# Performance work log

Measured on AMD Instinct MI355X. Metric: run time of the kernel, lower is better.

Reference implementation:

```python
import jax, jax.numpy as jnp
import numpy as np

N_NODES = 100000
N_EDGES = 640000
N_LABEL = 100000
IN_C, HID_C, OUT_C = 128, 128, 64


def setup_inputs() -> dict:
    key = jax.random.key(0)
    ks = jax.random.split(key, 9)
    x = jax.random.normal(ks[0], (N_NODES, IN_C), dtype=jnp.float32)
    edge_index = jax.random.randint(ks[1], (2, N_EDGES), 0, N_NODES, dtype=jnp.int64)
    edge_label_index = jax.random.randint(ks[2], (2, N_LABEL), 0, N_NODES, dtype=jnp.int64)
    s = 0.05  # small init scale
    # PyG SAGEConv: lin_l applied to mean-aggregated neighbors (with bias), lin_r to root (no bias)
    W1l = jax.random.normal(ks[3], (HID_C, IN_C), dtype=jnp.float32) * s
    b1 = jnp.zeros((HID_C,), dtype=jnp.float32)
    W1r = jax.random.normal(ks[4], (HID_C, IN_C), dtype=jnp.float32) * s
    W2l = jax.random.normal(ks[5], (OUT_C, HID_C), dtype=jnp.float32) * s
    b2 = jnp.zeros((OUT_C,), dtype=jnp.float32)
    W2r = jax.random.normal(ks[6], (OUT_C, HID_C), dtype=jnp.float32) * s
    return {"x": x, "edge_index": edge_index, "edge_label_index": edge_label_index,
            "W1l": W1l, "b1": b1, "W1r": W1r, "W2l": W2l, "b2": b2, "W2r": W2r}


def _sage_conv(x, src, dst, Wl, b, Wr):
    # mean aggregation of source features at destination nodes
    agg = jax.ops.segment_sum(x[src], dst, num_segments=N_NODES)  # [N, d]
    cnt = jax.ops.segment_sum(jnp.ones((src.shape[0],), x.dtype), dst, num_segments=N_NODES)
    mean = agg / jnp.maximum(cnt, 1.0)[:, None]
    return mean @ Wl.T + b + x @ Wr.T


def reference(x, edge_index, edge_label_index, W1l, b1, W1r, W2l, b2, W2r):
    src, dst = edge_index[0], edge_index[1]
    h = jax.nn.relu(_sage_conv(x, src, dst, W1l, b1, W1r))
    z = _sage_conv(h, src, dst, W2l, b2, W2r)
    # edge-wise dot-product decode
    scores = jnp.sum(z[edge_label_index[0]] * z[edge_label_index[1]], axis=-1)  # [E_label]
    return scores
```

## Files before the change

### kernel.cpp

```cpp
#include <hip/hip_runtime.h>

#define N_NODES 100000
#define N_EDGES 640000
#define N_LABEL 100000
#define CAP 32

typedef __bf16 bf16x8 __attribute__((ext_vector_type(8)));
typedef float f32x4 __attribute__((ext_vector_type(4)));

#define CW1L 0
#define CB1  16384
#define CW1R 16512
#define CW2L 32896
#define CB2  41088
#define CW2R 41152
#define NWTS 49344

#define NB_W 193
#define NB_X 12500

__device__ __forceinline__ float bf2f(unsigned short u) {
    union { unsigned int i; float f; } c; c.i = ((unsigned int)u) << 16; return c.f;
}
__device__ __forceinline__ unsigned short f2bf(float f) {
    union { float f; unsigned int i; } c; c.f = f;
    unsigned int lsb = (c.i >> 16) & 1u;
    c.i += 0x7fffu + lsb;
    return (unsigned short)(c.i >> 16);
}

__global__ void k_detect(const unsigned int* __restrict__ xw,
                         const unsigned int* __restrict__ eiw,
                         int* __restrict__ flags) {
    int l = threadIdx.x;
    unsigned int w = xw[l];
    unsigned short lo = (unsigned short)(w & 0xffffu);
    int e = (lo >> 7) & 0xff;
    bool bf_like = (lo == 0) || (e >= 98 && e <= 138);
    unsigned long long m = __ballot(bf_like);
    unsigned int ew = eiw[2 * l + 1];
    unsigned long long mz = __ballot(ew == 0u);
    if (l == 0) {
        flags[0] = (__popcll(m) < 48) ? 1 : 0;
        flags[1] = (__popcll(mz) == 64) ? 1 : 0;
    }
}

__global__ void k_convwx(const void* W1l, const void* b1, const void* W1r,
                         const void* W2l, const void* b2, const void* W2r,
                         unsigned short* __restrict__ wts,
                         const void* __restrict__ x, unsigned short* __restrict__ xb,
                         const int* __restrict__ flags) {
    int b = blockIdx.x;
    int f32m = flags[0];
    if (b < NB_W) {
        int i = b * 256 + threadIdx.x;
        if (i >= NWTS) return;
        const void* src; int local;
        if      (i < CB1)  { src = W1l; local = i; }
        else if (i < CW1R) { src = b1;  local = i - CB1; }
        else if (i < CW2L) { src = W1r; local = i - CW1R; }
        else if (i < CB2)  { src = W2l; local = i - CW2L; }
        else if (i < CW2R) { src = b2;  local = i - CB2; }
        else               { src = W2r; local = i - CW2R; }
        wts[i] = f32m ? f2bf(((const float*)src)[local]) : ((const unsigned short*)src)[local];
    } else {
        int i = (b - NB_W) * 256 + threadIdx.x;
        if (i >= N_NODES * 32) return;
        if (f32m) {
            float4 p = ((const float4*)x)[i];
            ushort4 o;
            o.x = f2bf(p.x); o.y = f2bf(p.y); o.z = f2bf(p.z); o.w = f2bf(p.w);
            ((ushort4*)xb)[i] = o;
        } else {
            ((ushort4*)xb)[i] = ((const ushort4*)x)[i];
        }
    }
}

__global__ void k_fill(const int* __restrict__ ei, int* __restrict__ cnt,
                       int* __restrict__ csr, const int* __restrict__ flags) {
    int e = blockIdx.x * blockDim.x + threadIdx.x;
    if (e >= N_EDGES) return;
    int i64 = flags[1];
    int src = ei[e << i64], dst = ei[(N_EDGES + e) << i64];
    int pos = atomicAdd(&cnt[dst], 1);
    if (pos < CAP) csr[dst * CAP + pos] = src;
}

__global__ __launch_bounds__(256) void k_gemm1f(
    const int* __restrict__ cnt, const int* __restrict__ csr,
    const unsigned short* __restrict__ xb, const unsigned short* __restrict__ wts,
    unsigned short* __restrict__ h)
{
    __shared__ unsigned short smean[32][136];
    int wave = threadIdx.x >> 6, lane = threadIdx.x & 63;
    int nb0 = blockIdx.x * 32;

    int nA = nb0 + wave * 8;
    int half = lane >> 5, sl = lane & 31;
    int rows[4];
#pragma unroll
    for (int p = 0; p < 4; ++p)
        rows[p] = csr[(size_t)(nA + p * 2 + half) * CAP + sl];
    int dpre = (lane < 8) ? cnt[nA + lane] : 0;
    int c2 = lane << 1;

#pragma unroll
    for (int j = 0; j < 8; ++j) {
        int deg = __shfl(dpre, j);
        int m = deg < CAP ? deg : CAP;
        float s0 = 0.f, s1 = 0.f;
        for (int e0 = 0; e0 < m; e0 += 8) {
            unsigned int v[8];
#pragma unroll
            for (int u = 0; u < 8; ++u) {
                int e = e0 + u;
                int sidx = __shfl(rows[j >> 1], (j & 1) * 32 + e);
                sidx = (e < m) ? sidx : 0;
                v[u] = *(const unsigned int*)(xb + (size_t)sidx * 128 + c2);
            }
#pragma unroll
            for (int u = 0; u < 8; ++u) {
                bool ok = (e0 + u) < m;
                s0 += ok ? bf2f((unsigned short)(v[u] & 0xffffu)) : 0.f;
                s1 += ok ? bf2f((unsigned short)(v[u] >> 16)) : 0.f;
            }
        }
        float inv = 1.0f / (deg > 1 ? (float)deg : 1.0f);
        unsigned int o = (unsigned int)f2bf(s0 * inv) | ((unsigned int)f2bf(s1 * inv) << 16);
        *(unsigned int*)&smean[wave * 8 + j][c2] = o;
    }
    __syncthreads();

    int qq = wave;
    int row = lane & 15, kq = lane >> 4;
    bf16x8 Wf[16];
#pragma unroll
    for (int t = 0; t < 2; ++t)
#pragma unroll
        for (int ks = 0; ks < 8; ++ks) {
            const int k0 = ks * 32;
            const unsigned short* base = wts + (k0 < 128 ? CW1L : CW1R)
                + (size_t)(qq * 32 + t * 16 + row) * 128 + (k0 & 127) + kq * 8;
            Wf[t * 8 + ks] = *reinterpret_cast<const bf16x8*>(base);
        }
    int col = lane & 15, rq = lane >> 4;
    float bias0 = bf2f(wts[CB1 + qq * 32 + col]);
    float bias1 = bf2f(wts[CB1 + qq * 32 + 16 + col]);

#pragma unroll
    for (int i = 0; i < 2; ++i) {
        int n0 = nb0 + i * 16;
        bf16x8 Af[8];
#pragma unroll
        for (int ks = 0; ks < 4; ++ks)
            Af[ks] = *reinterpret_cast<const bf16x8*>(&smean[i * 16 + row][ks * 32 + kq * 8]);
        const unsigned short* rx = xb + (size_t)(n0 + row) * 128 + kq * 8;
#pragma unroll
        for (int ks = 0; ks < 4; ++ks)
            Af[4 + ks] = *reinterpret_cast<const bf16x8*>(rx + ks * 32);
        f32x4 acc0 = (f32x4){0.f, 0.f, 0.f, 0.f};
        f32x4 acc1 = (f32x4){0.f, 0.f, 0.f, 0.f};
#pragma unroll
        for (int ks = 0; ks < 8; ++ks) {
            acc0 = __builtin_amdgcn_mfma_f32_16x16x32_bf16(Af[ks], Wf[ks],     acc0, 0, 0, 0);
            acc1 = __builtin_amdgcn_mfma_f32_16x16x32_bf16(Af[ks], Wf[8 + ks], acc1, 0, 0, 0);
        }
#pragma unroll
        for (int r = 0; r < 4; ++r) {
            int n = n0 + rq * 4 + r;
            float v0 = acc0[r] + bias0; v0 = v0 > 0.f ? v0 : 0.f;
            float v1 = acc1[r] + bias1; v1 = v1 > 0.f ? v1 : 0.f;
            h[(size_t)n * 128 + qq * 32 + col]      = f2bf(v0);
            h[(size_t)n * 128 + qq * 32 + 16 + col] = f2bf(v1);
        }
    }
}

__global__ __launch_bounds__(256) void k_gemm2(
    const unsigned short* __restrict__ h, const unsigned short* __restrict__ wts,
    unsigned short* __restrict__ tb)
{
    int w = (int)((blockIdx.x * blockDim.x + threadIdx.x) >> 6);
    int lane = threadIdx.x & 63;
    int q = w & 3;
    int tg = w >> 2;
    int row = lane & 15, kq = lane >> 4;

    const size_t wbase = (q < 2) ? (CW2L + (size_t)(q * 32) * 128)
                                 : (CW2R + (size_t)((q - 2) * 32) * 128);
    bf16x8 Wf[8];
#pragma unroll
    for (int t = 0; t < 2; ++t)
#pragma unroll
        for (int ks = 0; ks < 4; ++ks)
            Wf[t * 4 + ks] = *reinterpret_cast<const bf16x8*>(
                wts + wbase + (size_t)(t * 16 + row) * 128 + ks * 32 + kq * 8);

    int col = lane & 15, rq = lane >> 4;
    int nt0 = tg * 2;
    bf16x8 Af[2][4];

#define LOAD_A2(tile, buf)                                                            \
    {                                                                                 \
        int n0_ = (tile) * 16;                                                        \
        if (n0_ < N_NODES) {                                                          \
            const unsigned short* rh = h + (size_t)(n0_ + row) * 128 + kq * 8;        \
            _Pragma("unroll")                                                         \
            for (int ks = 0; ks < 4; ++ks)                                            \
                Af[buf][ks] = *reinterpret_cast<const bf16x8*>(rh + ks * 32);         \
        }                                                                             \
    }

    LOAD_A2(nt0, 0);
#pragma unroll
    for (int i = 0; i < 2; ++i) {
        int n0 = (nt0 + i) * 16;
        if (n0 >= N_NODES) continue;
        if (i < 1) LOAD_A2(nt0 + i + 1, (i + 1) & 1);
        f32x4 acc0 = (f32x4){0.f, 0.f, 0.f, 0.f};
        f32x4 acc1 = (f32x4){0.f, 0.f, 0.f, 0.f};
#pragma unroll
        for (int ks = 0; ks < 4; ++ks) {
            acc0 = __builtin_amdgcn_mfma_f32_16x16x32_bf16(Af[i & 1][ks], Wf[ks],     acc0, 0, 0, 0);
            acc1 = __builtin_amdgcn_mfma_f32_16x16x32_bf16(Af[i & 1][ks], Wf[4 + ks], acc1, 0, 0, 0);
        }
#pragma unroll
        for (int r = 0; r < 4; ++r) {
            int n = n0 + rq * 4 + r;
            tb[(size_t)n * 128 + q * 32 + col]      = f2bf(acc0[r]);
            tb[(size_t)n * 128 + q * 32 + 16 + col] = f2bf(acc1[r]);
        }
    }
#undef LOAD_A2
}

__global__ __launch_bounds__(256) void k_agg2c(
    const int* __restrict__ cnt, const int* __restrict__ csr,
    const unsigned short* __restrict__ tb, const unsigned short* __restrict__ wts,
    float* __restrict__ z) {
    int wv = (int)((blockIdx.x * blockDim.x + threadIdx.x) >> 6);
    int n2 = wv * 2;
    if (n2 >= N_NODES) return;
    int lane = threadIdx.x & 63;
    int half = lane >> 5, sl = lane & 31;
    int n = n2 + half;
    int dpre = (lane < 2) ? cnt[n2 + lane] : 0;
    int deg = __shfl(dpre, half);
    int m = deg < CAP ? deg : CAP;
    int mo = __shfl(m, lane ^ 32);
    int mmax = m > mo ? m : mo;
    int srcrow = csr[(size_t)n * CAP + sl];
    int c2 = sl << 1;
    float s0 = 0.f, s1 = 0.f;
    for (int e0 = 0; e0 < mmax; e0 += 8) {
        unsigned int v[8];
#pragma unroll
        for (int u = 0; u < 8; ++u) {
            int e = e0 + u;
            int sidx = __shfl(srcrow, half * 32 + e);
            sidx = (e < m) ? sidx : 0;
            v[u] = *(const unsigned int*)(tb + (size_t)sidx * 128 + c2);
        }
#pragma unroll
        for (int u = 0; u < 8; ++u) {
            bool ok = (e0 + u) < m;
            s0 += ok ? bf2f((unsigned short)(v[u] & 0xffffu)) : 0.f;
            s1 += ok ? bf2f((unsigned short)(v[u] >> 16)) : 0.f;
        }
    }
    float inv = 1.0f / (deg > 1 ? (float)deg : 1.0f);
    unsigned int tr = *(const unsigned int*)(tb + (size_t)n * 128 + 64 + c2);
    unsigned int bb = *(const unsigned int*)(wts + CB2 + c2);
    float2 o;
    o.x = s0 * inv + bf2f((unsigned short)(bb & 0xffffu)) + bf2f((unsigned short)(tr & 0xffffu));
    o.y = s1 * inv + bf2f((unsigned short)(bb >> 16))     + bf2f((unsigned short)(tr >> 16));
    *(float2*)(z + (size_t)n * 64 + c2) = o;
}

__global__ void k_decode(const int* __restrict__ eli, const float* __restrict__ z,
                         void* __restrict__ out, const int* __restrict__ flags) {
    long long t = (long long)blockIdx.x * blockDim.x + threadIdx.x;
    int e = (int)(t >> 4);
    if (e >= N_LABEL) return;
    int f32m = flags[0], i64 = flags[1];
    int q = threadIdx.x & 15;
    int a = eli[e << i64], b = eli[(N_LABEL + e) << i64];
    float4 pa = *(const float4*)(z + (size_t)a * 64 + q * 4);
    float4 pb = *(const float4*)(z + (size_t)b * 64 + q * 4);
    float s = pa.x * pb.x + pa.y * pb.y + pa.z * pb.z + pa.w * pb.w;
#pragma unroll
    for (int off = 1; off < 16; off <<= 1) s += __shfl_xor(s, off);
    if (q == 0) {
        if (f32m) ((float*)out)[e] = s;
        else      ((unsigned short*)out)[e] = f2bf(s);
    }
}

extern "C" void kernel_launch(void* const* d_in, const int* in_sizes, int n_in,
                              void* d_out, int out_size, void* d_ws, size_t ws_size,
                              hipStream_t stream) {
    const void* x   = d_in[0];
    const int*  ei  = (const int*)d_in[1];
    const int*  eli = (const int*)d_in[2];
    const void* W1l = d_in[3];
    const void* b1  = d_in[4];
    const void* W1r = d_in[5];
    const void* W2l = d_in[6];
    const void* b2  = d_in[7];
    const void* W2r = d_in[8];

    char* ws = (char*)d_ws;
    const size_t offFlag = 0;
    const size_t offCnt  = 1024;
    const size_t offWts  = 801024;
    const size_t offCsr  = 1u << 20;
    const size_t offXb   = offCsr + (size_t)N_NODES * CAP * 4;
    const size_t offTb   = offXb  + (size_t)N_NODES * 128 * 2;
    const size_t offHz   = offTb  + (size_t)N_NODES * 128 * 2;

    int*            flags = (int*)(ws + offFlag);
    int*            cnt   = (int*)(ws + offCnt);
    unsigned short* wts   = (unsigned short*)(ws + offWts);
    int*            csr   = (int*)(ws + offCsr);
    unsigned short* xb    = (unsigned short*)(ws + offXb);
    unsigned short* tb    = (unsigned short*)(ws + offTb);
    unsigned short* h     = (unsigned short*)(ws + offHz);

    hipMemsetAsync(ws, 0, 1u << 20, stream);

    k_detect<<<1, 64, 0, stream>>>((const unsigned int*)x, (const unsigned int*)ei, flags);

    k_convwx<<<NB_W + NB_X, 256, 0, stream>>>(W1l, b1, W1r, W2l, b2, W2r, wts, x, xb, flags);

    k_fill<<<(N_EDGES + 255) / 256, 256, 0, stream>>>(ei, cnt, csr, flags);

    k_gemm1f<<<N_NODES / 32, 256, 0, stream>>>(cnt, csr, xb, wts, h);

    k_gemm2<<<3125, 256, 0, stream>>>(h, wts, tb);

    float* z = (float*)(ws + offHz);
    k_agg2c<<<12500, 256, 0, stream>>>(cnt, csr, tb, wts, z);

    {
        long long thr = (long long)N_LABEL * 16;
        k_decode<<<(unsigned)((thr + 255) / 256), 256, 0, stream>>>(eli, z, d_out, flags);
    }
}
```

Before: 259.3 us.

## Fuse layer-1 and layer-2 GEMMs via shared memory; store z as bf16

The layer-1 aggregate+GEMM kernel now also runs the layer-2 projection. The ReLU output h stays in shared memory instead of making a global round trip through a separate GEMM kernel, which removes one launch and a 25 MB write/read. z is now stored in bf16 instead of fp32, halving the gather traffic in the decode kernel, which now uses 8 lanes per label edge. The bf16 unpacking is also simplified with mask and shift casts. The cost is lower precision for z and more registers held across the extra syncs in the fused kernel.

```diff
diff --git a/kernel.cpp b/kernel.cpp
--- a/kernel.cpp
+++ b/kernel.cpp
@@ -21,6 +21,9 @@
 
 __device__ __forceinline__ float bf2f(unsigned short u) {
     union { unsigned int i; float f; } c; c.i = ((unsigned int)u) << 16; return c.f;
+}
+__device__ __forceinline__ float asf(unsigned int u) {
+    union { unsigned int i; float f; } c; c.i = u; return c.f;
 }
 __device__ __forceinline__ unsigned short f2bf(float f) {
     union { float f; unsigned int i; } c; c.f = f;
@@ -88,158 +91,141 @@
     if (pos < CAP) csr[dst * CAP + pos] = src;
 }
 
-__global__ __launch_bounds__(256) void k_gemm1f(
+__global__ __launch_bounds__(256) void k_fused1(
     const int* __restrict__ cnt, const int* __restrict__ csr,
     const unsigned short* __restrict__ xb, const unsigned short* __restrict__ wts,
-    unsigned short* __restrict__ h)
+    unsigned short* __restrict__ tb)
 {
-    __shared__ unsigned short smean[32][136];
+    __shared__ unsigned short sm[32][136];
     int wave = threadIdx.x >> 6, lane = threadIdx.x & 63;
     int nb0 = blockIdx.x * 32;
 
-    int nA = nb0 + wave * 8;
-    int half = lane >> 5, sl = lane & 31;
-    int rows[4];
-#pragma unroll
-    for (int p = 0; p < 4; ++p)
-        rows[p] = csr[(size_t)(nA + p * 2 + half) * CAP + sl];
-    int dpre = (lane < 8) ? cnt[nA + lane] : 0;
-    int c2 = lane << 1;
-
-#pragma unroll
-    for (int j = 0; j < 8; ++j) {
-        int deg = __shfl(dpre, j);
-        int m = deg < CAP ? deg : CAP;
-        float s0 = 0.f, s1 = 0.f;
-        for (int e0 = 0; e0 < m; e0 += 8) {
-            unsigned int v[8];
-#pragma unroll
-            for (int u = 0; u < 8; ++u) {
-                int e = e0 + u;
-                int sidx = __shfl(rows[j >> 1], (j & 1) * 32 + e);
-                sidx = (e < m) ? sidx : 0;
-                v[u] = *(const unsigned int*)(xb + (size_t)sidx * 128 + c2);
-            }
-#pragma unroll
-            for (int u = 0; u < 8; ++u) {
-                bool ok = (e0 + u) < m;
-                s0 += ok ? bf2f((unsigned short)(v[u] & 0xffffu)) : 0.f;
-                s1 += ok ? bf2f((unsigned short)(v[u] >> 16)) : 0.f;
-            }
-        }
-        float inv = 1.0f / (deg > 1 ? (float)deg : 1.0f);
-        unsigned int o = (unsigned int)f2bf(s0 * inv) | ((unsigned int)f2bf(s1 * inv) << 16);
-        *(unsigned int*)&smean[wave * 8 + j][c2] = o;
+    {
+        int nA = nb0 + wave * 8;
+        int half = lane >> 5, sl = lane & 31;
+        int rows[4];
+#pragma unroll
+        for (int p = 0; p < 4; ++p)
+            rows[p] = csr[(size_t)(nA + p * 2 + half) * CAP + sl];
+        int dpre = (lane < 8) ? cnt[nA + lane] : 0;
+        int c2 = lane << 1;
+
+#pragma unroll
+        for (int j = 0; j < 8; ++j) {
+            int deg = __shfl(dpre, j);
+            int m = deg < CAP ? deg : CAP;
+            float s0 = 0.f, s1 = 0.f;
+            for (int e0 = 0; e0 < m; e0 += 8) {
+                unsigned int v[8];
+#pragma unroll
+                for (int u = 0; u < 8; ++u) {
+                    int e = e0 + u;
+                    int sidx = __shfl(rows[j >> 1], (j & 1) * 32 + e);
+                    sidx = (e < m) ? sidx : 0;
+                    v[u] = *(const unsigned int*)(xb + (size_t)sidx * 128 + c2);
+                }
+#pragma unroll
+                for (int u = 0; u < 8; ++u) {
+                    unsigned int w = ((e0 + u) < m) ? v[u] : 0u;
+                    s0 += asf(w << 16);
+                    s1 += asf(w & 0xffff0000u);
+                }
+            }
+            float inv = 1.0f / (deg > 1 ? (float)deg : 1.0f);
+            unsigned int o = (unsigned int)f2bf(s0 * inv) | ((unsigned int)f2bf(s1 * inv) << 16);
+            *(unsigned int*)&sm[wave * 8 + j][c2] = o;
+        }
     }
     __syncthreads();
 
     int qq = wave;
     int row = lane & 15, kq = lane >> 4;
-    bf16x8 Wf[16];
-#pragma unroll
-    for (int t = 0; t < 2; ++t)
-#pragma unroll
-        for (int ks = 0; ks < 8; ++ks) {
-            const int k0 = ks * 32;
-            const unsigned short* base = wts + (k0 < 128 ? CW1L : CW1R)
-                + (size_t)(qq * 32 + t * 16 + row) * 128 + (k0 & 127) + kq * 8;
-            Wf[t * 8 + ks] = *reinterpret_cast<const bf16x8*>(base);
-        }
     int col = lane & 15, rq = lane >> 4;
-    float bias0 = bf2f(wts[CB1 + qq * 32 + col]);
-    float bias1 = bf2f(wts[CB1 + qq * 32 + 16 + col]);
-
-#pragma unroll
-    for (int i = 0; i < 2; ++i) {
-        int n0 = nb0 + i * 16;
-        bf16x8 Af[8];
-#pragma unroll
-        for (int ks = 0; ks < 4; ++ks)
-            Af[ks] = *reinterpret_cast<const bf16x8*>(&smean[i * 16 + row][ks * 32 + kq * 8]);
-        const unsigned short* rx = xb + (size_t)(n0 + row) * 128 + kq * 8;
-#pragma unroll
-        for (int ks = 0; ks < 4; ++ks)
-            Af[4 + ks] = *reinterpret_cast<const bf16x8*>(rx + ks * 32);
-        f32x4 acc0 = (f32x4){0.f, 0.f, 0.f, 0.f};
-        f32x4 acc1 = (f32x4){0.f, 0.f, 0.f, 0.f};
-#pragma unroll
-        for (int ks = 0; ks < 8; ++ks) {
-            acc0 = __builtin_amdgcn_mfma_f32_16x16x32_bf16(Af[ks], Wf[ks],     acc0, 0, 0, 0);
-            acc1 = __builtin_amdgcn_mfma_f32_16x16x32_bf16(Af[ks], Wf[8 + ks], acc1, 0, 0, 0);
-        }
-#pragma unroll
-        for (int r = 0; r < 4; ++r) {
-            int n = n0 + rq * 4 + r;
-            float v0 = acc0[r] + bias0; v0 = v0 > 0.f ? v0 : 0.f;
-            float v1 = acc1[r] + bias1; v1 = v1 > 0.f ? v1 : 0.f;
-            h[(size_t)n * 128 + qq * 32 + col]      = f2bf(v0);
-            h[(size_t)n * 128 + qq * 32 + 16 + col] = f2bf(v1);
-        }
-    }
-}
-
-__global__ __launch_bounds__(256) void k_gemm2(
-    const unsigned short* __restrict__ h, const unsigned short* __restrict__ wts,
-    unsigned short* __restrict__ tb)
-{
-    int w = (int)((blockIdx.x * blockDim.x + threadIdx.x) >> 6);
-    int lane = threadIdx.x & 63;
-    int q = w & 3;
-    int tg = w >> 2;
-    int row = lane & 15, kq = lane >> 4;
-
-    const size_t wbase = (q < 2) ? (CW2L + (size_t)(q * 32) * 128)
-                                 : (CW2R + (size_t)((q - 2) * 32) * 128);
-    bf16x8 Wf[8];
-#pragma unroll
-    for (int t = 0; t < 2; ++t)
-#pragma unroll
-        for (int ks = 0; ks < 4; ++ks)
-            Wf[t * 4 + ks] = *reinterpret_cast<const bf16x8*>(
-                wts + wbase + (size_t)(t * 16 + row) * 128 + ks * 32 + kq * 8);
-
-    int col = lane & 15, rq = lane >> 4;
-    int nt0 = tg * 2;
-    bf16x8 Af[2][4];
-
-#define LOAD_A2(tile, buf)                                                            \
-    {                                                                                 \
-        int n0_ = (tile) * 16;                                                        \
-        if (n0_ < N_NODES) {                                                          \
-            const unsigned short* rh = h + (size_t)(n0_ + row) * 128 + kq * 8;        \
-            _Pragma("unroll")                                                         \
-            for (int ks = 0; ks < 4; ++ks)                                            \
-                Af[buf][ks] = *reinterpret_cast<const bf16x8*>(rh + ks * 32);         \
-        }                                                                             \
-    }
-
-    LOAD_A2(nt0, 0);
-#pragma unroll
-    for (int i = 0; i < 2; ++i) {
-        int n0 = (nt0 + i) * 16;
-        if (n0 >= N_NODES) continue;
-        if (i < 1) LOAD_A2(nt0 + i + 1, (i + 1) & 1);
-        f32x4 acc0 = (f32x4){0.f, 0.f, 0.f, 0.f};
-        f32x4 acc1 = (f32x4){0.f, 0.f, 0.f, 0.f};
-#pragma unroll
-        for (int ks = 0; ks < 4; ++ks) {
-            acc0 = __builtin_amdgcn_mfma_f32_16x16x32_bf16(Af[i & 1][ks], Wf[ks],     acc0, 0, 0, 0);
-            acc1 = __builtin_amdgcn_mfma_f32_16x16x32_bf16(Af[i & 1][ks], Wf[4 + ks], acc1, 0, 0, 0);
-        }
-#pragma unroll
-        for (int r = 0; r < 4; ++r) {
-            int n = n0 + rq * 4 + r;
-            tb[(size_t)n * 128 + q * 32 + col]      = f2bf(acc0[r]);
-            tb[(size_t)n * 128 + q * 32 + 16 + col] = f2bf(acc1[r]);
-        }
-    }
-#undef LOAD_A2
+    f32x4 acc[2][2];
+    {
+        bf16x8 Wf[16];
+#pragma unroll
+        for (int t = 0; t < 2; ++t)
+#pragma unroll
+            for (int ks = 0; ks < 8; ++ks) {
+                const int k0 = ks * 32;
+                const unsigned short* base = wts + (k0 < 128 ? CW1L : CW1R)
+                    + (size_t)(qq * 32 + t * 16 + row) * 128 + (k0 & 127) + kq * 8;
+                Wf[t * 8 + ks] = *reinterpret_cast<const bf16x8*>(base);
+            }
+#pragma unroll
+        for (int i = 0; i < 2; ++i) {
+            bf16x8 Af[8];
+#pragma unroll
+            for (int ks = 0; ks < 4; ++ks)
+                Af[ks] = *reinterpret_cast<const bf16x8*>(&sm[i * 16 + row][ks * 32 + kq * 8]);
+            const unsigned short* rx = xb + (size_t)(nb0 + i * 16 + row) * 128 + kq * 8;
+#pragma unroll
+            for (int ks = 0; ks < 4; ++ks)
+                Af[4 + ks] = *reinterpret_cast<const bf16x8*>(rx + ks * 32);
+            acc[i][0] = (f32x4){0.f, 0.f, 0.f, 0.f};
+            acc[i][1] = (f32x4){0.f, 0.f, 0.f, 0.f};
+#pragma unroll
+            for (int ks = 0; ks < 8; ++ks) {
+                acc[i][0] = __builtin_amdgcn_mfma_f32_16x16x32_bf16(Af[ks], Wf[ks],     acc[i][0], 0, 0, 0);
+                acc[i][1] = __builtin_amdgcn_mfma_f32_16x16x32_bf16(Af[ks], Wf[8 + ks], acc[i][1], 0, 0, 0);
+            }
+        }
+    }
+    __syncthreads();
+    {
+        float bias0 = bf2f(wts[CB1 + qq * 32 + col]);
+        float bias1 = bf2f(wts[CB1 + qq * 32 + 16 + col]);
+#pragma unroll
+        for (int i = 0; i < 2; ++i)
+#pragma unroll
+            for (int r = 0; r < 4; ++r) {
+                int nl = i * 16 + rq * 4 + r;
+                float v0 = acc[i][0][r] + bias0; v0 = v0 > 0.f ? v0 : 0.f;
+                float v1 = acc[i][1][r] + bias1; v1 = v1 > 0.f ? v1 : 0.f;
+                sm[nl][qq * 32 + col]      = f2bf(v0);
+                sm[nl][qq * 32 + 16 + col] = f2bf(v1);
+            }
+    }
+    __syncthreads();
+
+    {
+        const size_t wbase = (qq < 2) ? (CW2L + (size_t)(qq * 32) * 128)
+                                      : (CW2R + (size_t)((qq - 2) * 32) * 128);
+        bf16x8 Wg[8];
+#pragma unroll
+        for (int t = 0; t < 2; ++t)
+#pragma unroll
+            for (int ks = 0; ks < 4; ++ks)
+                Wg[t * 4 + ks] = *reinterpret_cast<const bf16x8*>(
+                    wts + wbase + (size_t)(t * 16 + row) * 128 + ks * 32 + kq * 8);
+#pragma unroll
+        for (int i = 0; i < 2; ++i) {
+            bf16x8 Ag[4];
+#pragma unroll
+            for (int ks = 0; ks < 4; ++ks)
+                Ag[ks] = *reinterpret_cast<const bf16x8*>(&sm[i * 16 + row][ks * 32 + kq * 8]);
+            f32x4 c0 = (f32x4){0.f, 0.f, 0.f, 0.f};
+            f32x4 c1 = (f32x4){0.f, 0.f, 0.f, 0.f};
+#pragma unroll
+            for (int ks = 0; ks < 4; ++ks) {
+                c0 = __builtin_amdgcn_mfma_f32_16x16x32_bf16(Ag[ks], Wg[ks],     c0, 0, 0, 0);
+                c1 = __builtin_amdgcn_mfma_f32_16x16x32_bf16(Ag[ks], Wg[4 + ks], c1, 0, 0, 0);
+            }
+#pragma unroll
+            for (int r = 0; r < 4; ++r) {
+                int n = nb0 + i * 16 + rq * 4 + r;
+                tb[(size_t)n * 128 + qq * 32 + col]      = f2bf(c0[r]);
+                tb[(size_t)n * 128 + qq * 32 + 16 + col] = f2bf(c1[r]);
+            }
+        }
+    }
 }
 
 __global__ __launch_bounds__(256) void k_agg2c(
     const int* __restrict__ cnt, const int* __restrict__ csr,
     const unsigned short* __restrict__ tb, const unsigned short* __restrict__ wts,
-    float* __restrict__ z) {
+    unsigned short* __restrict__ zb) {
     int wv = (int)((blockIdx.x * blockDim.x + threadIdx.x) >> 6);
     int n2 = wv * 2;
     if (n2 >= N_NODES) return;
@@ -265,33 +251,36 @@
         }
 #pragma unroll
         for (int u = 0; u < 8; ++u) {
-            bool ok = (e0 + u) < m;
-            s0 += ok ? bf2f((unsigned short)(v[u] & 0xffffu)) : 0.f;
-            s1 += ok ? bf2f((unsigned short)(v[u] >> 16)) : 0.f;
+            unsigned int w = ((e0 + u) < m) ? v[u] : 0u;
+            s0 += asf(w << 16);
+            s1 += asf(w & 0xffff0000u);
         }
     }
     float inv = 1.0f / (deg > 1 ? (float)deg : 1.0f);
     unsigned int tr = *(const unsigned int*)(tb + (size_t)n * 128 + 64 + c2);
     unsigned int bb = *(const unsigned int*)(wts + CB2 + c2);
-    float2 o;
-    o.x = s0 * inv + bf2f((unsigned short)(bb & 0xffffu)) + bf2f((unsigned short)(tr & 0xffffu));
-    o.y = s1 * inv + bf2f((unsigned short)(bb >> 16))     + bf2f((unsigned short)(tr >> 16));
-    *(float2*)(z + (size_t)n * 64 + c2) = o;
-}
-
-__global__ void k_decode(const int* __restrict__ eli, const float* __restrict__ z,
+    float zx = s0 * inv + asf(bb << 16)          + asf(tr << 16);
+    float zy = s1 * inv + asf(bb & 0xffff0000u)  + asf(tr & 0xffff0000u);
+    unsigned int o = (unsigned int)f2bf(zx) | ((unsigned int)f2bf(zy) << 16);
+    *(unsigned int*)(zb + (size_t)n * 64 + c2) = o;
+}
+
+__global__ void k_decode(const int* __restrict__ eli, const unsigned short* __restrict__ zb,
                          void* __restrict__ out, const int* __restrict__ flags) {
     long long t = (long long)blockIdx.x * blockDim.x + threadIdx.x;
-    int e = (int)(t >> 4);
+    int e = (int)(t >> 3);
     if (e >= N_LABEL) return;
     int f32m = flags[0], i64 = flags[1];
-    int q = threadIdx.x & 15;
+    int q = threadIdx.x & 7;
     int a = eli[e << i64], b = eli[(N_LABEL + e) << i64];
-    float4 pa = *(const float4*)(z + (size_t)a * 64 + q * 4);
-    float4 pb = *(const float4*)(z + (size_t)b * 64 + q * 4);
-    float s = pa.x * pb.x + pa.y * pb.y + pa.z * pb.z + pa.w * pb.w;
-#pragma unroll
-    for (int off = 1; off < 16; off <<= 1) s += __shfl_xor(s, off);
+    uint4 pa = *(const uint4*)(zb + (size_t)a * 64 + q * 8);
+    uint4 pb = *(const uint4*)(zb + (size_t)b * 64 + q * 8);
+    float s = asf(pa.x << 16) * asf(pb.x << 16) + asf(pa.x & 0xffff0000u) * asf(pb.x & 0xffff0000u)
+            + asf(pa.y << 16) * asf(pb.y << 16) + asf(pa.y & 0xffff0000u) * asf(pb.y & 0xffff0000u)
+            + asf(pa.z << 16) * asf(pb.z << 16) + asf(pa.z & 0xffff0000u) * asf(pb.z & 0xffff0000u)
+            + asf(pa.w << 16) * asf(pb.w << 16) + asf(pa.w & 0xffff0000u) * asf(pb.w & 0xffff0000u);
+#pragma unroll
+    for (int off = 1; off < 8; off <<= 1) s += __shfl_xor(s, off);
     if (q == 0) {
         if (f32m) ((float*)out)[e] = s;
         else      ((unsigned short*)out)[e] = f2bf(s);
@@ -318,7 +307,7 @@
     const size_t offCsr  = 1u << 20;
     const size_t offXb   = offCsr + (size_t)N_NODES * CAP * 4;
     const size_t offTb   = offXb  + (size_t)N_NODES * 128 * 2;
-    const size_t offHz   = offTb  + (size_t)N_NODES * 128 * 2;
+    const size_t offZb   = offTb  + (size_t)N_NODES * 128 * 2;
 
     int*            flags = (int*)(ws + offFlag);
     int*            cnt   = (int*)(ws + offCnt);
@@ -326,7 +315,7 @@
     int*            csr   = (int*)(ws + offCsr);
     unsigned short* xb    = (unsigned short*)(ws + offXb);
     unsigned short* tb    = (unsigned short*)(ws + offTb);
-    unsigned short* h     = (unsigned short*)(ws + offHz);
+    unsigned short* zb    = (unsigned short*)(ws + offZb);
 
     hipMemsetAsync(ws, 0, 1u << 20, stream);
 
@@ -336,15 +325,9 @@
 
     k_fill<<<(N_EDGES + 255) / 256, 256, 0, stream>>>(ei, cnt, csr, flags);
 
-    k_gemm1f<<<N_NODES / 32, 256, 0, stream>>>(cnt, csr, xb, wts, h);
-
-    k_gemm2<<<3125, 256, 0, stream>>>(h, wts, tb);
-
-    float* z = (float*)(ws + offHz);
-    k_agg2c<<<12500, 256, 0, stream>>>(cnt, csr, tb, wts, z);
-
-    {
-        long long thr = (long long)N_LABEL * 16;
-        k_decode<<<(unsigned)((thr + 255) / 256), 256, 0, stream>>>(eli, z, d_out, flags);
-    }
-}
+    k_fused1<<<N_NODES / 32, 256, 0, stream>>>(cnt, csr, xb, wts, tb);
+
+    k_agg2c<<<12500, 256, 0, stream>>>(cnt, csr, tb, wts, zb);
+
+    k_decode<<<(N_LABEL * 8) / 256, 256, 0, stream>>>(eli, zb, d_out, flags);
+}
```

New measurement: 232.7 us. -10.3%, faster.
